# Kernel tuning notes

Hardware: AMD Instinct MI355X
Metric: run time of the kernel (lower is better)

Reference implementation:

```python
import jax, jax.numpy as jnp
import numpy as np

SOS_TOKEN = 1
MAX_LENGTH = 64
VOCAB = 32000
HIDDEN = 1024
BATCH = 32


def setup_inputs() -> dict:
    key = jax.random.key(0)
    ks = jax.random.split(key, 10)
    s = 1.0 / np.sqrt(HIDDEN)
    return {
        "encoder_outputs": jax.random.normal(ks[0], (BATCH, MAX_LENGTH, HIDDEN), dtype=jnp.float32),
        "encoder_hidden": jax.random.normal(ks[1], (1, BATCH, HIDDEN), dtype=jnp.float32),
        "target_tensor": jax.random.randint(ks[2], (BATCH, MAX_LENGTH), 0, VOCAB),
        "embedding": jax.random.normal(ks[3], (VOCAB, HIDDEN), dtype=jnp.float32),
        "W_ih": jax.random.uniform(ks[4], (3 * HIDDEN, HIDDEN), jnp.float32, -s, s),
        "W_hh": jax.random.uniform(ks[5], (3 * HIDDEN, HIDDEN), jnp.float32, -s, s),
        "b_ih": jax.random.uniform(ks[6], (3 * HIDDEN,), jnp.float32, -s, s),
        "b_hh": jax.random.uniform(ks[7], (3 * HIDDEN,), jnp.float32, -s, s),
        "out_W": jax.random.uniform(ks[8], (VOCAB, HIDDEN), jnp.float32, -s, s),
        "out_b": jax.random.uniform(ks[9], (VOCAB,), jnp.float32, -s, s),
    }


def _decode(encoder_hidden, target_tensor, embedding, W_ih, W_hh, b_ih, b_hh, out_W, out_b):
    B = target_tensor.shape[0]
    # teacher forcing: input at step i is SOS (i=0) else target[:, i-1]
    sos = jnp.full((B, 1), SOS_TOKEN, dtype=target_tensor.dtype)
    inputs = jnp.concatenate([sos, target_tensor[:, :-1]], axis=1)  # [B,T]
    x = jax.nn.relu(embedding[inputs])  # [B,T,H]
    # precompute all input-side gate projections in one GEMM: [B,T,3H]
    xg = jnp.einsum("bth,gh->btg", x, W_ih) + b_ih
    h0 = encoder_hidden[0]  # [B,H]

    def step(h, xg_t):
        hg = h @ W_hh.T + b_hh  # [B,3H]
        xr, xz, xn = jnp.split(xg_t, 3, axis=-1)
        hr, hz, hn = jnp.split(hg, 3, axis=-1)
        r = jax.nn.sigmoid(xr + hr)
        z = jax.nn.sigmoid(xz + hz)
        n = jnp.tanh(xn + r * hn)
        h_new = (1.0 - z) * n + z * h
        return h_new, h_new

    h_last, hs = jax.lax.scan(step, h0, jnp.swapaxes(xg, 0, 1))
    hs = jnp.swapaxes(hs, 0, 1)  # [B,T,H]
    logits = jnp.einsum("bth,vh->btv", hs, out_W) + out_b
    log_probs = jax.nn.log_softmax(logits, axis=-1)
    return log_probs, h_last[None]  # hidden shaped [1,B,H] like torch GRU


def reference(encoder_outputs, encoder_hidden, target_tensor, embedding, W_ih, W_hh, b_ih, b_hh, out_W, out_b):
    del encoder_outputs  # only used for batch size in the original
    return _decode(encoder_hidden, target_tensor, embedding, W_ih, W_hh, b_ih, b_hh, out_W, out_b)
```

## Files before the change

### kernel.cpp

```cpp
#include <hip/hip_runtime.h>
#include <hip/hip_bf16.h>

#define B_ 32
#define T_ 64
#define H_ 1024
#define G3 3072
#define V_ 32000
#define M_ 2048
#define NB_SCAN 64

typedef __attribute__((ext_vector_type(8))) short s16x8;
typedef __attribute__((ext_vector_type(4))) float f32x4;
typedef __bf16 bf16x8 __attribute__((ext_vector_type(8)));

__device__ inline unsigned short f2bf(float f) {
    union { float f; unsigned int u; } v; v.f = f;
    unsigned int u = v.u;
    return (unsigned short)((u + 0x7FFFu + ((u >> 16) & 1u)) >> 16);
}

__global__ void cast_f32_bf16(const float* __restrict__ src, unsigned short* __restrict__ dst, int n) {
    int i = (blockIdx.x * blockDim.x + threadIdx.x) * 4;
    int stride = gridDim.x * blockDim.x * 4;
    for (; i < n; i += stride) {
        float4 v = *(const float4*)(src + i);
        ushort4 o;
        o.x = f2bf(v.x); o.y = f2bf(v.y); o.z = f2bf(v.z); o.w = f2bf(v.w);
        *(ushort4*)(dst + i) = o;
    }
}

__global__ void embed_relu(const int* __restrict__ target, const float* __restrict__ emb,
                           unsigned short* __restrict__ x) {
    int m = blockIdx.x;
    int b = m >> 6, t = m & 63;
    int tok = (t == 0) ? 1 : target[b * T_ + t - 1];
    const float* row = emb + (size_t)tok * H_;
    int k = threadIdx.x * 4;
    float4 v = *(const float4*)(row + k);
    ushort4 o;
    o.x = f2bf(fmaxf(v.x, 0.f)); o.y = f2bf(fmaxf(v.y, 0.f));
    o.z = f2bf(fmaxf(v.z, 0.f)); o.w = f2bf(fmaxf(v.w, 0.f));
    *(ushort4*)(x + (size_t)m * H_ + k) = o;
}

__global__ void init_h(const float* __restrict__ enc_hidden,
                       float* __restrict__ hf, unsigned short* __restrict__ hb) {
    int i = blockIdx.x * blockDim.x + threadIdx.x;
    if (i < B_ * H_) {
        float v = enc_hidden[i];
        hf[i] = v;
        hb[i] = f2bf(v);
    }
}

__global__ void zero_u32(unsigned int* __restrict__ p, int n) {
    int i = blockIdx.x * blockDim.x + threadIdx.x;
    if (i < n) p[i] = 0;
}

__global__ __launch_bounds__(256) void gemm_bias(
    const unsigned short* __restrict__ A,
    const unsigned short* __restrict__ Bm,
    const float* __restrict__ bias,
    float* __restrict__ C,
    int N, int K)
{
    __shared__ __align__(16) unsigned short As[2 * 4096];
    __shared__ __align__(16) unsigned short Bs[2 * 4096];
    int n0 = blockIdx.x * 128, m0 = blockIdx.y * 128;
    int tid = threadIdx.x;
    int lane = tid & 63, wv = tid >> 6;
    int wr = wv >> 1, wc = wv & 1;

    f32x4 acc[4][4] = {};

    int o0 = wv * 2048 + lane * 16;
    int row0 = o0 >> 6, ib0 = (o0 & 63) >> 1;
    int o1 = o0 + 1024;
    int row1 = o1 >> 6, ib1 = (o1 & 63) >> 1;

    auto stage = [&](int buf, int k0) {
        const unsigned short* ga0 = A + (size_t)(m0 + row0) * K + k0 + ib0;
        const unsigned short* gb0 = Bm + (size_t)(n0 + row0) * K + k0 + ib0;
        const unsigned short* ga1 = A + (size_t)(m0 + row1) * K + k0 + ib1;
        const unsigned short* gb1 = Bm + (size_t)(n0 + row1) * K + k0 + ib1;
        unsigned short* la0 = As + buf * 4096 + wv * 1024;
        unsigned short* lb0 = Bs + buf * 4096 + wv * 1024;
        __builtin_amdgcn_global_load_lds((const __attribute__((address_space(1))) void*)ga0,
                                         (__attribute__((address_space(3))) void*)la0, 16, 0, 0);
        __builtin_amdgcn_global_load_lds((const __attribute__((address_space(1))) void*)gb0,
                                         (__attribute__((address_space(3))) void*)lb0, 16, 0, 0);
        __builtin_amdgcn_global_load_lds((const __attribute__((address_space(1))) void*)ga1,
                                         (__attribute__((address_space(3))) void*)(la0 + 512), 16, 0, 0);
        __builtin_amdgcn_global_load_lds((const __attribute__((address_space(1))) void*)gb1,
                                         (__attribute__((address_space(3))) void*)(lb0 + 512), 16, 0, 0);
    };

    int kq = (lane >> 4) * 8;
    int rA = wr * 64 + (lane & 15);
    int rB = wc * 64 + (lane & 15);

    int NT = K >> 5;
    stage(0, 0);
    __syncthreads();

    int cur = 0;
    for (int t = 0; t < NT; ++t) {
        if (t + 1 < NT) stage(cur ^ 1, (t + 1) << 5);
        const unsigned short* ab = As + cur * 4096;
        const unsigned short* bb = Bs + cur * 4096;
        s16x8 af[4], bf[4];
#pragma unroll
        for (int i = 0; i < 4; ++i) {
            af[i] = *(const s16x8*)(ab + (rA + i * 16) * 32 + kq);
            bf[i] = *(const s16x8*)(bb + (rB + i * 16) * 32 + kq);
        }
#pragma unroll
        for (int mf = 0; mf < 4; ++mf)
#pragma unroll
            for (int nf = 0; nf < 4; ++nf)
                acc[mf][nf] = __builtin_amdgcn_mfma_f32_16x16x32_bf16(
                    __builtin_bit_cast(bf16x8, af[mf]),
                    __builtin_bit_cast(bf16x8, bf[nf]),
                    acc[mf][nf], 0, 0, 0);
        __syncthreads();
        cur ^= 1;
    }

#pragma unroll
    for (int nf = 0; nf < 4; ++nf) {
        int col = n0 + wc * 64 + nf * 16 + (lane & 15);
        float bv = bias[col];
#pragma unroll
        for (int mf = 0; mf < 4; ++mf) {
            int mbase = m0 + wr * 64 + mf * 16 + (lane >> 4) * 4;
#pragma unroll
            for (int r = 0; r < 4; ++r)
                C[(size_t)(mbase + r) * N + col] = acc[mf][nf][r] + bv;
        }
    }
}

__global__ __launch_bounds__(256) void gru_scan(
    const unsigned short* __restrict__ Whhb,
    const float* __restrict__ b_hh,
    const float* __restrict__ xg,
    unsigned short* __restrict__ hb0, unsigned short* __restrict__ hb1,
    float* __restrict__ hf0, float* __restrict__ hf1,
    unsigned short* __restrict__ hs,
    unsigned int* __restrict__ ctr)
{
    __shared__ __align__(16) unsigned short ws_[48 * 1024];
    __shared__ __align__(16) f32x4 red[2][3][64];

    int tid = threadIdx.x;
    int lane = tid & 63, wave = tid >> 6;
    int rt = wave >> 1, kh = wave & 1;
    int ct = blockIdx.x;

    for (int idx = tid; idx < 48 * 128; idx += 256) {
        int r = idx >> 7, slot = idx & 127;
        int g = r >> 4, jr = r & 15;
        s16x8 v = *(const s16x8*)(Whhb + (size_t)(g * H_ + ct * 16 + jr) * H_ + slot * 8);
        *(s16x8*)(ws_ + r * 1024 + (slot ^ (r & 7)) * 8) = v;
    }
    __syncthreads();

    int rr = lane & 15, q = lane >> 4;
    int col = ct * 16 + rr;
    int xsw = rr & 7;
    int kbase = kh * 512;
    int sbase = kh * 64 + q;
    float br = b_hh[col], bz = b_hh[H_ + col], bn = b_hh[2 * H_ + col];
    int b0 = rt * 16 + q * 4;

    for (int t = 0; t < T_; ++t) {
        const unsigned short* hbp = (t & 1) ? hb1 : hb0;
        const float*          hfp = (t & 1) ? hf1 : hf0;
        unsigned short*       hbn = (t & 1) ? hb0 : hb1;
        float*                hfn = (t & 1) ? hf0 : hf1;

        float xr[4], xz[4], xn[4], hold[4];
        if (kh == 1) {
#pragma unroll
            for (int r = 0; r < 4; ++r) {
                int b = b0 + r;
                const float* xrow = xg + ((size_t)b * T_ + t) * G3;
                xr[r] = xrow[col]; xz[r] = xrow[H_ + col]; xn[r] = xrow[2 * H_ + col];
                hold[r] = hfp[b * H_ + col];
            }
        }

        f32x4 accr, accz, accn;
        if (kh == 1) {
            accr = (f32x4){br, br, br, br};
            accz = (f32x4){bz, bz, bz, bz};
            accn = (f32x4){bn, bn, bn, bn};
        } else {
            accr = (f32x4){0.f, 0.f, 0.f, 0.f};
            accz = accr; accn = accr;
        }

        const unsigned short* ha = hbp + (size_t)(rt * 16 + rr) * H_ + kbase + q * 8;
#pragma unroll 8
        for (int kk = 0; kk < 512; kk += 32) {
            s16x8 af = *(const s16x8*)(ha + kk);
            int so = ((sbase + (kk >> 3)) ^ xsw) * 8;
            s16x8 fr = *(const s16x8*)(ws_ + rr * 1024 + so);
            s16x8 fz = *(const s16x8*)(ws_ + (16 + rr) * 1024 + so);
            s16x8 fn = *(const s16x8*)(ws_ + (32 + rr) * 1024 + so);
            bf16x8 a = __builtin_bit_cast(bf16x8, af);
            accr = __builtin_amdgcn_mfma_f32_16x16x32_bf16(a, __builtin_bit_cast(bf16x8, fr), accr, 0, 0, 0);
            accz = __builtin_amdgcn_mfma_f32_16x16x32_bf16(a, __builtin_bit_cast(bf16x8, fz), accz, 0, 0, 0);
            accn = __builtin_amdgcn_mfma_f32_16x16x32_bf16(a, __builtin_bit_cast(bf16x8, fn), accn, 0, 0, 0);
        }

        if (kh == 0) {
            red[rt][0][lane] = accr; red[rt][1][lane] = accz; red[rt][2][lane] = accn;
        }
        __syncthreads();
        if (kh == 1) {
            accr += red[rt][0][lane]; accz += red[rt][1][lane]; accn += red[rt][2][lane];
#pragma unroll
            for (int r = 0; r < 4; ++r) {
                int b = b0 + r;
                float rg = 1.f / (1.f + __expf(-(xr[r] + accr[r])));
                float zg = 1.f / (1.f + __expf(-(xz[r] + accz[r])));
                float ng = tanhf(xn[r] + rg * accn[r]);
                float hnew = (1.f - zg) * ng + zg * hold[r];
                hfn[b * H_ + col] = hnew;
                unsigned short h16 = f2bf(hnew);
                hbn[b * H_ + col] = h16;
                hs[((size_t)b * T_ + t) * H_ + col] = h16;
            }
        }

        if (t < T_ - 1) {
            __syncthreads();
            if (tid == 0) {
                __builtin_amdgcn_fence(__ATOMIC_RELEASE, "agent");
                __hip_atomic_fetch_add(&ctr[t], 1u, __ATOMIC_RELEASE, __HIP_MEMORY_SCOPE_AGENT);
                while (__hip_atomic_load(&ctr[t], __ATOMIC_ACQUIRE, __HIP_MEMORY_SCOPE_AGENT) < (unsigned)NB_SCAN)
                    __builtin_amdgcn_s_sleep(2);
                __builtin_amdgcn_fence(__ATOMIC_ACQUIRE, "agent");
            }
            __syncthreads();
        }
    }
}

__global__ __launch_bounds__(256) void log_softmax_inplace(float* __restrict__ out) {
    int m = blockIdx.x;
    float* row = out + (size_t)m * V_;
    int tid = threadIdx.x;
    __shared__ float sm[4], ss[4];

    float mx = -1e30f, s = 0.f;
    for (int i = tid * 4; i < V_; i += 1024) {
        float4 v = *(const float4*)(row + i);
        float lm = fmaxf(fmaxf(v.x, v.y), fmaxf(v.z, v.w));
        float ns = __expf(v.x - lm) + __expf(v.y - lm) + __expf(v.z - lm) + __expf(v.w - lm);
        if (lm > mx) { s = s * __expf(mx - lm) + ns; mx = lm; }
        else          { s += ns * __expf(lm - mx); }
    }
    for (int o = 32; o > 0; o >>= 1) {
        float om = __shfl_xor(mx, o), os = __shfl_xor(s, o);
        float nm = fmaxf(mx, om);
        s = s * __expf(mx - nm) + os * __expf(om - nm);
        mx = nm;
    }
    int wv = tid >> 6, lane = tid & 63;
    if (lane == 0) { sm[wv] = mx; ss[wv] = s; }
    __syncthreads();
    float fm = fmaxf(fmaxf(sm[0], sm[1]), fmaxf(sm[2], sm[3]));
    float fs = ss[0] * __expf(sm[0] - fm) + ss[1] * __expf(sm[1] - fm)
             + ss[2] * __expf(sm[2] - fm) + ss[3] * __expf(sm[3] - fm);
    float lse = fm + __logf(fs);

    for (int i = tid * 4; i < V_; i += 1024) {
        float4 v = *(const float4*)(row + i);
        v.x -= lse; v.y -= lse; v.z -= lse; v.w -= lse;
        *(float4*)(row + i) = v;
    }
}

__global__ void copy_f32(const float* __restrict__ src, float* __restrict__ dst, int n) {
    int i = blockIdx.x * blockDim.x + threadIdx.x;
    if (i < n) dst[i] = src[i];
}

extern "C" void kernel_launch(void* const* d_in, const int* in_sizes, int n_in,
                              void* d_out, int out_size, void* d_ws, size_t ws_size,
                              hipStream_t stream) {
    const float* enc_hidden = (const float*)d_in[1];
    const int*   target     = (const int*)d_in[2];
    const float* embedding  = (const float*)d_in[3];
    const float* W_ih       = (const float*)d_in[4];
    const float* W_hh       = (const float*)d_in[5];
    const float* b_ih       = (const float*)d_in[6];
    const float* b_hh       = (const float*)d_in[7];
    const float* out_W      = (const float*)d_in[8];
    const float* out_b      = (const float*)d_in[9];
    float* out = (float*)d_out;

    char* ws = (char*)d_ws;
    float*          xg   = (float*)(ws);
    unsigned short* xb   = (unsigned short*)(ws + 25165824);
    unsigned short* hsb  = (unsigned short*)(ws + 29360128);
    unsigned short* wihb = (unsigned short*)(ws + 33554432);
    unsigned short* whhb = (unsigned short*)(ws + 39845888);
    unsigned short* owb  = (unsigned short*)(ws + 46137344);
    float*          hf0  = (float*)(ws + 111673344);
    float*          hf1  = (float*)(ws + 111804416);
    unsigned short* hb0  = (unsigned short*)(ws + 111935488);
    unsigned short* hb1  = (unsigned short*)(ws + 112001024);
    unsigned int*   ctr  = (unsigned int*)(ws + 112066560);

    cast_f32_bf16<<<512, 256, 0, stream>>>(W_ih, wihb, G3 * H_);
    cast_f32_bf16<<<512, 256, 0, stream>>>(W_hh, whhb, G3 * H_);
    cast_f32_bf16<<<2048, 256, 0, stream>>>(out_W, owb, V_ * H_);
    embed_relu<<<M_, 256, 0, stream>>>(target, embedding, xb);
    init_h<<<128, 256, 0, stream>>>(enc_hidden, hf0, hb0);
    zero_u32<<<1, 64, 0, stream>>>(ctr, 64);

    gemm_bias<<<dim3(G3 / 128, M_ / 128), 256, 0, stream>>>(xb, wihb, b_ih, xg, G3, H_);

    {
        void* args[] = { (void*)&whhb, (void*)&b_hh, (void*)&xg,
                         (void*)&hb0, (void*)&hb1, (void*)&hf0, (void*)&hf1,
                         (void*)&hsb, (void*)&ctr };
        hipLaunchCooperativeKernel((const void*)gru_scan, dim3(NB_SCAN), dim3(256), args, 0, stream);
    }

    gemm_bias<<<dim3(V_ / 128, M_ / 128), 256, 0, stream>>>(hsb, owb, out_b, out, V_, H_);
    log_softmax_inplace<<<M_, 256, 0, stream>>>(out);
    copy_f32<<<128, 256, 0, stream>>>(hf0, out + (size_t)M_ * V_, B_ * H_);
}
```

Baseline: 1.034 ms.

## Replace atomic-counter grid barrier with per-block flags and cache-bypassing hidden-state exchange

Reworks the recurrent scan's cross-block synchronisation. Each block now publishes its step number to its own flag with a cache-coherent store, and every wave polls all 64 flags, replacing the single-thread atomic counter, fences and extra block barrier. The hidden state stays in registers in fp32 across steps instead of round-tripping through global memory. All 16 A-fragment loads are issued up front with sc0/sc1 coherent loads, and bf16 outputs are packed in pairs via a lane shuffle so stores are 32-bit. This targets per-step latency in the 64 serial steps, but it depends on hand-written inline asm for cache coherence and on every wave polling the flags.

```diff
diff --git a/kernel.cpp b/kernel.cpp
--- a/kernel.cpp
+++ b/kernel.cpp
@@ -17,6 +17,20 @@
     union { float f; unsigned int u; } v; v.f = f;
     unsigned int u = v.u;
     return (unsigned short)((u + 0x7FFFu + ((u >> 16) & 1u)) >> 16);
+}
+
+__device__ inline s16x8 load_b128_cc(const void* p) {
+    s16x8 r;
+    asm volatile("global_load_dwordx4 %0, %1, off sc0 sc1" : "=v"(r) : "v"(p));
+    return r;
+}
+__device__ inline unsigned int load_b32_cc(const void* p) {
+    unsigned int r;
+    asm volatile("global_load_dword %0, %1, off sc0 sc1" : "=v"(r) : "v"(p));
+    return r;
+}
+__device__ inline void store_b32_cc(void* p, unsigned int v) {
+    asm volatile("global_store_dword %0, %1, off sc0 sc1" :: "v"(p), "v"(v) : "memory");
 }
 
 __global__ void cast_f32_bf16(const float* __restrict__ src, unsigned short* __restrict__ dst, int n) {
@@ -44,14 +58,9 @@
     *(ushort4*)(x + (size_t)m * H_ + k) = o;
 }
 
-__global__ void init_h(const float* __restrict__ enc_hidden,
-                       float* __restrict__ hf, unsigned short* __restrict__ hb) {
+__global__ void init_h(const float* __restrict__ enc_hidden, unsigned short* __restrict__ hb) {
     int i = blockIdx.x * blockDim.x + threadIdx.x;
-    if (i < B_ * H_) {
-        float v = enc_hidden[i];
-        hf[i] = v;
-        hb[i] = f2bf(v);
-    }
+    if (i < B_ * H_) hb[i] = f2bf(enc_hidden[i]);
 }
 
 __global__ void zero_u32(unsigned int* __restrict__ p, int n) {
@@ -145,11 +154,12 @@
 __global__ __launch_bounds__(256) void gru_scan(
     const unsigned short* __restrict__ Whhb,
     const float* __restrict__ b_hh,
+    const float* __restrict__ enc_hidden,
     const float* __restrict__ xg,
     unsigned short* __restrict__ hb0, unsigned short* __restrict__ hb1,
-    float* __restrict__ hf0, float* __restrict__ hf1,
+    float* __restrict__ hfF,
     unsigned short* __restrict__ hs,
-    unsigned int* __restrict__ ctr)
+    unsigned int* __restrict__ flags)
 {
     __shared__ __align__(16) unsigned short ws_[48 * 1024];
     __shared__ __align__(16) f32x4 red[2][3][64];
@@ -175,20 +185,27 @@
     float br = b_hh[col], bz = b_hh[H_ + col], bn = b_hh[2 * H_ + col];
     int b0 = rt * 16 + q * 4;
 
+    float hold[4];
+    if (kh == 1) {
+#pragma unroll
+        for (int r = 0; r < 4; ++r) hold[r] = enc_hidden[(b0 + r) * H_ + col];
+    }
+
     for (int t = 0; t < T_; ++t) {
         const unsigned short* hbp = (t & 1) ? hb1 : hb0;
-        const float*          hfp = (t & 1) ? hf1 : hf0;
         unsigned short*       hbn = (t & 1) ? hb0 : hb1;
-        float*                hfn = (t & 1) ? hf0 : hf1;
-
-        float xr[4], xz[4], xn[4], hold[4];
+
+        const unsigned short* ha = hbp + (size_t)(rt * 16 + rr) * H_ + kbase + q * 8;
+        s16x8 af[16];
+#pragma unroll
+        for (int i = 0; i < 16; ++i) af[i] = load_b128_cc(ha + i * 32);
+
+        float xr[4], xz[4], xn[4];
         if (kh == 1) {
 #pragma unroll
             for (int r = 0; r < 4; ++r) {
-                int b = b0 + r;
-                const float* xrow = xg + ((size_t)b * T_ + t) * G3;
+                const float* xrow = xg + ((size_t)(b0 + r) * T_ + t) * G3;
                 xr[r] = xrow[col]; xz[r] = xrow[H_ + col]; xn[r] = xrow[2 * H_ + col];
-                hold[r] = hfp[b * H_ + col];
             }
         }
 
@@ -202,15 +219,16 @@
             accz = accr; accn = accr;
         }
 
-        const unsigned short* ha = hbp + (size_t)(rt * 16 + rr) * H_ + kbase + q * 8;
-#pragma unroll 8
-        for (int kk = 0; kk < 512; kk += 32) {
-            s16x8 af = *(const s16x8*)(ha + kk);
-            int so = ((sbase + (kk >> 3)) ^ xsw) * 8;
+        asm volatile("s_waitcnt vmcnt(0)");
+        __builtin_amdgcn_sched_barrier(0);
+
+#pragma unroll
+        for (int kk = 0; kk < 16; ++kk) {
+            int so = ((sbase + kk * 4) ^ xsw) * 8;
             s16x8 fr = *(const s16x8*)(ws_ + rr * 1024 + so);
             s16x8 fz = *(const s16x8*)(ws_ + (16 + rr) * 1024 + so);
             s16x8 fn = *(const s16x8*)(ws_ + (32 + rr) * 1024 + so);
-            bf16x8 a = __builtin_bit_cast(bf16x8, af);
+            bf16x8 a = __builtin_bit_cast(bf16x8, af[kk]);
             accr = __builtin_amdgcn_mfma_f32_16x16x32_bf16(a, __builtin_bit_cast(bf16x8, fr), accr, 0, 0, 0);
             accz = __builtin_amdgcn_mfma_f32_16x16x32_bf16(a, __builtin_bit_cast(bf16x8, fz), accz, 0, 0, 0);
             accn = __builtin_amdgcn_mfma_f32_16x16x32_bf16(a, __builtin_bit_cast(bf16x8, fn), accn, 0, 0, 0);
@@ -222,30 +240,44 @@
         __syncthreads();
         if (kh == 1) {
             accr += red[rt][0][lane]; accz += red[rt][1][lane]; accn += red[rt][2][lane];
+            unsigned int hpk[4];
 #pragma unroll
             for (int r = 0; r < 4; ++r) {
-                int b = b0 + r;
                 float rg = 1.f / (1.f + __expf(-(xr[r] + accr[r])));
                 float zg = 1.f / (1.f + __expf(-(xz[r] + accz[r])));
                 float ng = tanhf(xn[r] + rg * accn[r]);
                 float hnew = (1.f - zg) * ng + zg * hold[r];
-                hfn[b * H_ + col] = hnew;
-                unsigned short h16 = f2bf(hnew);
-                hbn[b * H_ + col] = h16;
-                hs[((size_t)b * T_ + t) * H_ + col] = h16;
-            }
+                hold[r] = hnew;
+                hpk[r] = f2bf(hnew);
+            }
+#pragma unroll
+            for (int r = 0; r < 4; ++r) {
+                unsigned int other = __shfl_xor((int)hpk[r], 1);
+                if ((rr & 1) == 0) {
+                    unsigned int pk = hpk[r] | (other << 16);
+                    size_t e = (size_t)(b0 + r) * H_ + col;
+                    store_b32_cc(hbn + e, pk);
+                    *(unsigned int*)(hs + ((size_t)(b0 + r) * T_ + t) * H_ + col) = pk;
+                }
+            }
+            if (t == T_ - 1) {
+#pragma unroll
+                for (int r = 0; r < 4; ++r) hfF[(b0 + r) * H_ + col] = hold[r];
+            }
+            asm volatile("s_waitcnt vmcnt(0)" ::: "memory");
         }
 
         if (t < T_ - 1) {
             __syncthreads();
-            if (tid == 0) {
-                __builtin_amdgcn_fence(__ATOMIC_RELEASE, "agent");
-                __hip_atomic_fetch_add(&ctr[t], 1u, __ATOMIC_RELEASE, __HIP_MEMORY_SCOPE_AGENT);
-                while (__hip_atomic_load(&ctr[t], __ATOMIC_ACQUIRE, __HIP_MEMORY_SCOPE_AGENT) < (unsigned)NB_SCAN)
-                    __builtin_amdgcn_s_sleep(2);
-                __builtin_amdgcn_fence(__ATOMIC_ACQUIRE, "agent");
-            }
-            __syncthreads();
+            if (tid == 0) store_b32_cc(flags + ct, (unsigned int)(t + 1));
+            unsigned int tgt = (unsigned int)(t + 1);
+            while (true) {
+                unsigned int f = load_b32_cc(flags + lane);
+                asm volatile("s_waitcnt vmcnt(0)");
+                if (__all(f >= tgt)) break;
+                __builtin_amdgcn_s_sleep(1);
+            }
+            __builtin_amdgcn_sched_barrier(0);
         }
     }
 }
@@ -311,29 +343,27 @@
     unsigned short* wihb = (unsigned short*)(ws + 33554432);
     unsigned short* whhb = (unsigned short*)(ws + 39845888);
     unsigned short* owb  = (unsigned short*)(ws + 46137344);
-    float*          hf0  = (float*)(ws + 111673344);
-    float*          hf1  = (float*)(ws + 111804416);
-    unsigned short* hb0  = (unsigned short*)(ws + 111935488);
-    unsigned short* hb1  = (unsigned short*)(ws + 112001024);
-    unsigned int*   ctr  = (unsigned int*)(ws + 112066560);
+    float*          hfF  = (float*)(ws + 111673344);
+    unsigned short* hb0  = (unsigned short*)(ws + 111804416);
+    unsigned short* hb1  = (unsigned short*)(ws + 111869952);
+    unsigned int*   flg  = (unsigned int*)(ws + 111935488);
 
     cast_f32_bf16<<<512, 256, 0, stream>>>(W_ih, wihb, G3 * H_);
     cast_f32_bf16<<<512, 256, 0, stream>>>(W_hh, whhb, G3 * H_);
     cast_f32_bf16<<<2048, 256, 0, stream>>>(out_W, owb, V_ * H_);
     embed_relu<<<M_, 256, 0, stream>>>(target, embedding, xb);
-    init_h<<<128, 256, 0, stream>>>(enc_hidden, hf0, hb0);
-    zero_u32<<<1, 64, 0, stream>>>(ctr, 64);
+    init_h<<<128, 256, 0, stream>>>(enc_hidden, hb0);
+    zero_u32<<<1, 64, 0, stream>>>(flg, 64);
 
     gemm_bias<<<dim3(G3 / 128, M_ / 128), 256, 0, stream>>>(xb, wihb, b_ih, xg, G3, H_);
 
     {
-        void* args[] = { (void*)&whhb, (void*)&b_hh, (void*)&xg,
-                         (void*)&hb0, (void*)&hb1, (void*)&hf0, (void*)&hf1,
-                         (void*)&hsb, (void*)&ctr };
+        void* args[] = { (void*)&whhb, (void*)&b_hh, (void*)&enc_hidden, (void*)&xg,
+                         (void*)&hb0, (void*)&hb1, (void*)&hfF, (void*)&hsb, (void*)&flg };
         hipLaunchCooperativeKernel((const void*)gru_scan, dim3(NB_SCAN), dim3(256), args, 0, stream);
     }
 
     gemm_bias<<<dim3(V_ / 128, M_ / 128), 256, 0, stream>>>(hsb, owb, out_b, out, V_, H_);
     log_softmax_inplace<<<M_, 256, 0, stream>>>(out);
-    copy_f32<<<128, 256, 0, stream>>>(hf0, out + (size_t)M_ * V_, B_ * H_);
-}
+    copy_f32<<<128, 256, 0, stream>>>(hfF, out + (size_t)M_ * V_, B_ * H_);
+}
```

New measurement: 936.9 us. 9.4% less time.
